# Optimization experiments

Hardware: AMD Instinct MI355X
Metric: run time of the kernel (lower is better)

Reference implementation:

```python
import jax, jax.numpy as jnp
import numpy as np

HEADS = 8
DIM_HEAD = 64
SCALE = DIM_HEAD ** -0.5


def setup_inputs() -> dict:
    key = jax.random.key(0)
    k1, k2, k3 = jax.random.split(key, 3)
    B, N, D = 4, 2048, HEADS * DIM_HEAD  # D = inner_dim = 512
    x = jax.random.normal(k1, (B, N, D), dtype=jnp.float32)
    # nn.Linear weights stored transposed vs torch; here we use [in, out]
    w_qkv = jax.random.normal(k2, (D, 3 * D), dtype=jnp.float32) * (D ** -0.5)
    w_out = jax.random.normal(k3, (D, D), dtype=jnp.float32) * (D ** -0.5)
    b_out = jnp.zeros((D,), dtype=jnp.float32)
    return {"x": x, "w_qkv": w_qkv, "w_out": w_out, "b_out": b_out}


def reference(x, w_qkv, w_out, b_out):
    B, N, D = x.shape
    qkv = x @ w_qkv  # [B, N, 3D]
    q, k, v = jnp.split(qkv, 3, axis=-1)

    def to_heads(t):  # b n (h d) -> b h n d
        return t.reshape(B, N, HEADS, DIM_HEAD).transpose(0, 2, 1, 3)

    q, k, v = to_heads(q), to_heads(k), to_heads(v)
    dots = jnp.einsum('bhnd,bhmd->bhnm', q, k) * SCALE  # [B,H,N,N]
    attn = jax.nn.softmax(dots, axis=-1)
    out = jnp.einsum('bhnm,bhmd->bhnd', attn, v)  # [B,H,N,d]
    out = out.transpose(0, 2, 1, 3).reshape(B, N, D)  # b h n d -> b n (h d)
    return out @ w_out + b_out
```

## Files before the change

kernel.cpp:

```cpp
#include <hip/hip_runtime.h>

typedef __bf16 bf16;
typedef __bf16 bf16x8 __attribute__((ext_vector_type(8)));
typedef __bf16 bf16x4 __attribute__((ext_vector_type(4)));
typedef float f32x4 __attribute__((ext_vector_type(4)));
typedef float f32x16 __attribute__((ext_vector_type(16)));

#define MFMA16(a, b, c) __builtin_amdgcn_mfma_f32_16x16x32_bf16(a, b, c, 0, 0, 0)
#define MFMA32(a, b, c) __builtin_amdgcn_mfma_f32_32x32x16_bf16(a, b, c, 0, 0, 0)

#define CS 0.18033688011112042f

#if __has_builtin(__builtin_amdgcn_exp2f)
#define EXP2(x) __builtin_amdgcn_exp2f(x)
#else
#define EXP2(x) exp2f(x)
#endif

__device__ __forceinline__ void load_lds16(const bf16* g, bf16* l) {
    __builtin_amdgcn_global_load_lds(
        (const __attribute__((address_space(1))) unsigned int*)g,
        (__attribute__((address_space(3))) unsigned int*)l, 16, 0, 0);
}

__device__ __forceinline__ bf16x4 shfl_xor32_b64(bf16x4 v) {
    union { bf16x4 b; int i[2]; } u;
    u.b = v;
    u.i[0] = __shfl_xor(u.i[0], 32, 64);
    u.i[1] = __shfl_xor(u.i[1], 32, 64);
    return u.b;
}

__device__ __forceinline__ bf16x8 build_bfrag(bf16x4 plo, bf16x4 phi, int h) {
    bf16x4 xlo = shfl_xor32_b64(plo);
    bf16x4 xhi = shfl_xor32_b64(phi);
    bf16x4 lo4 = h ? xhi : plo;
    bf16x4 hi4 = h ? phi : xlo;
    bf16x8 bb;
#pragma unroll
    for (int i = 0; i < 4; ++i) { bb[i] = lo4[i]; bb[4 + i] = hi4[i]; }
    return bb;
}

__global__ __launch_bounds__(256) void f32_to_bf16_kernel(const float* __restrict__ in,
                                                          bf16* __restrict__ out, int n) {
    int i = (blockIdx.x * 256 + threadIdx.x) * 4;
    if (i < n) {
        float4 v = *(const float4*)&in[i];
        bf16x4 o = {(bf16)v.x, (bf16)v.y, (bf16)v.z, (bf16)v.w};
        *(bf16x4*)&out[i] = o;
    }
}

__global__ __launch_bounds__(256) void transpose_f2b(const float* __restrict__ in,
                                                     bf16* __restrict__ out,
                                                     int R, int C) {
    __shared__ float tile[32][33];
    int tx = threadIdx.x & 31, ty = threadIdx.x >> 5;
    int c0 = blockIdx.x * 32, r0 = blockIdx.y * 32;
#pragma unroll
    for (int i = ty; i < 32; i += 8)
        tile[i][tx] = in[(size_t)(r0 + i) * C + c0 + tx];
    __syncthreads();
#pragma unroll
    for (int i = ty; i < 32; i += 8)
        out[(size_t)(c0 + i) * R + r0 + tx] = (bf16)tile[tx][i];
}

__global__ __launch_bounds__(256) void transpose_v_kernel(const bf16* __restrict__ qkv,
                                                          bf16* __restrict__ vt) {
    __shared__ bf16 tile[32][33];
    int tx = threadIdx.x & 31, ty = threadIdx.x >> 5;
    int bh = blockIdx.z, b = bh >> 3, h = bh & 7;
    int n0 = blockIdx.x * 32, d0 = blockIdx.y * 32;
#pragma unroll
    for (int i = ty; i < 32; i += 8)
        tile[i][tx] = qkv[(size_t)(b * 2048 + n0 + i) * 1536 + 1024 + h * 64 + d0 + tx];
    __syncthreads();
#pragma unroll
    for (int i = ty; i < 32; i += 8)
        vt[(size_t)(bh * 64 + d0 + i) * 2048 + n0 + tx] = tile[tx][i];
}

template <int MT, int MODE, typename OutT>
__global__ __launch_bounds__(256, 4) void gemm_bt_kernel(const bf16* __restrict__ A,
                                                         const bf16* __restrict__ Bt,
                                                         const float* __restrict__ bias,
                                                         OutT* __restrict__ C,
                                                         int M, int N, int K) {
    const int BM = MT * 32;
    __shared__ bf16 As[BM * 64];
    __shared__ bf16 Bs[128 * 64];
    int t = threadIdx.x;
    int lane = t & 63, w = t >> 6;
    int wr = w >> 1, wc = w & 1;
    int quad = lane >> 4, r16 = lane & 15;
    int m0 = blockIdx.y * BM, n0 = blockIdx.x * 128;

    const f32x4 fzero = {0.f, 0.f, 0.f, 0.f};
    f32x4 acc[MT][4];
#pragma unroll
    for (int i = 0; i < MT; ++i)
#pragma unroll
        for (int j = 0; j < 4; ++j) acc[i][j] = fzero;

    const bf16* ap[MT]; bf16* ad[MT];
    const bf16* bp[4];  bf16* bd[4];
#pragma unroll
    for (int i = 0; i < MT; ++i) {
        int ci = i * 256 + t;
        int row = ci >> 3, cp = ci & 7, cc = cp ^ (row & 7);
        ap[i] = &A[(size_t)(m0 + row) * K + cc * 8];
        ad[i] = &As[ci * 8];
    }
#pragma unroll
    for (int i = 0; i < 4; ++i) {
        int ci = i * 256 + t;
        int row = ci >> 3, cp = ci & 7, cc = cp ^ (row & 7);
        bp[i] = &Bt[(size_t)(n0 + row) * K + cc * 8];
        bd[i] = &Bs[ci * 8];
    }

    for (int k0 = 0; k0 < K; k0 += 64) {
        __syncthreads();
#pragma unroll
        for (int i = 0; i < MT; ++i) { load_lds16(ap[i], ad[i]); ap[i] += 64; }
#pragma unroll
        for (int i = 0; i < 4; ++i) { load_lds16(bp[i], bd[i]); bp[i] += 64; }
        __syncthreads();
#pragma unroll
        for (int ks = 0; ks < 2; ++ks) {
            bf16x8 af[MT], bfr[4];
            int cp = (ks * 4 + quad) ^ (r16 & 7);
#pragma unroll
            for (int mt = 0; mt < MT; ++mt)
                af[mt] = *(const bf16x8*)&As[(wr * (BM / 2) + mt * 16 + r16) * 64 + cp * 8];
#pragma unroll
            for (int nt = 0; nt < 4; ++nt)
                bfr[nt] = *(const bf16x8*)&Bs[(wc * 64 + nt * 16 + r16) * 64 + cp * 8];
#pragma unroll
            for (int mt = 0; mt < MT; ++mt)
#pragma unroll
                for (int nt = 0; nt < 4; ++nt)
                    acc[mt][nt] = MFMA16(af[mt], bfr[nt], acc[mt][nt]);
        }
    }
#pragma unroll
    for (int mt = 0; mt < MT; ++mt)
#pragma unroll
        for (int nt = 0; nt < 4; ++nt)
#pragma unroll
            for (int r = 0; r < 4; ++r) {
                int row = m0 + wr * (BM / 2) + mt * 16 + quad * 4 + r;
                int col = n0 + wc * 64 + nt * 16 + r16;
                float v = acc[mt][nt][r];
                if (MODE == 1 && n0 < 512) v *= CS;
                if (MODE == 2) v += bias[col];
                C[(size_t)row * N + col] = (OutT)v;
            }
}

__global__ __launch_bounds__(256, 2) void attn_kernel(const bf16* __restrict__ qkv,
                                                      const bf16* __restrict__ vt,
                                                      bf16* __restrict__ out) {
    __shared__ bf16 smem[16384];

    int t = threadIdx.x;
    int lane = t & 63, w = t >> 6;
    int h = lane >> 5, q = lane & 31;
    int g = w >> 1, wq = w & 1;
    int tt = t & 127;
    int bh = blockIdx.y, b = bh >> 3, hd = bh & 7;
    int qb = blockIdx.x * 64;
    int qrow = qb + wq * 32 + q;

    bf16x8 qf[4];
    {
        size_t qoff = (size_t)(b * 2048 + qrow) * 1536 + hd * 64;
#pragma unroll
        for (int s = 0; s < 4; ++s)
            qf[s] = *(const bf16x8*)&qkv[qoff + s * 16 + h * 8];
    }
    bf16x8 ones;
#pragma unroll
    for (int i = 0; i < 8; ++i) ones[i] = (bf16)1.0f;

    f32x16 o_acc[2], lacc;
#pragma unroll
    for (int i = 0; i < 16; ++i) { o_acc[0][i] = 0.f; o_acc[1][i] = 0.f; lacc[i] = 0.f; }

    bf16* Ks = &smem[g * 8192];
    bf16* Vs = Ks + 4096;

    const bf16* kp[4]; const bf16* vp[4];
    bf16* kd[4]; bf16* vd[4];
#pragma unroll
    for (int rdd = 0; rdd < 4; ++rdd) {
        int ci = rdd * 128 + tt;
        int row = ci >> 3, cp = ci & 7, cc = cp ^ (row & 7);
        kp[rdd] = &qkv[(size_t)(b * 2048 + g * 1024 + row) * 1536 + 512 + hd * 64 + cc * 8];
        kd[rdd] = &Ks[ci * 8];
        vp[rdd] = &vt[(size_t)(bh * 64 + row) * 2048 + g * 1024 + cc * 8];
        vd[rdd] = &Vs[ci * 8];
    }

    for (int it = 0; it < 16; ++it) {
        __syncthreads();
#pragma unroll
        for (int rdd = 0; rdd < 4; ++rdd) {
            load_lds16(kp[rdd], kd[rdd]); kp[rdd] += (size_t)64 * 1536;
            load_lds16(vp[rdd], vd[rdd]); vp[rdd] += 64;
        }
        __syncthreads();

        f32x16 sacc[2];
#pragma unroll
        for (int kb = 0; kb < 2; ++kb)
#pragma unroll
            for (int i = 0; i < 16; ++i) sacc[kb][i] = 0.f;

#pragma unroll
        for (int kb = 0; kb < 2; ++kb) {
            int m = kb * 32 + q;
#pragma unroll
            for (int s = 0; s < 4; ++s) {
                int cp = (s * 2 + h) ^ (q & 7);
                bf16x8 kf = *(const bf16x8*)&Ks[m * 64 + cp * 8];
                sacc[kb] = MFMA32(kf, qf[s], sacc[kb]);
            }
        }

        bf16x8 bfr[4];
#pragma unroll
        for (int kb = 0; kb < 2; ++kb) {
            bf16x4 pk[4];
#pragma unroll
            for (int g8 = 0; g8 < 4; ++g8)
#pragma unroll
                for (int i = 0; i < 4; ++i)
                    pk[g8][i] = (bf16)EXP2(sacc[kb][4 * g8 + i]);
#pragma unroll
            for (int wi = 0; wi < 2; ++wi)
                bfr[kb * 2 + wi] = build_bfrag(pk[2 * wi], pk[2 * wi + 1], h);
        }

#pragma unroll
        for (int j = 0; j < 4; ++j) lacc = MFMA32(ones, bfr[j], lacc);

#pragma unroll
        for (int kstep = 0; kstep < 4; ++kstep)
#pragma unroll
            for (int db = 0; db < 2; ++db) {
                int d = db * 32 + q;
                int cp = (kstep * 2 + h) ^ (q & 7);
                bf16x8 vf = *(const bf16x8*)&Vs[d * 64 + cp * 8];
                o_acc[db] = MFMA32(vf, bfr[kstep], o_acc[db]);
            }
    }

    float l_own = __shfl(lacc[0], q, 64);

    __syncthreads();
    float* Of = (float*)smem;
    float* Lf = (float*)(smem + 8192);
    bf16*  Ot = smem + 8320;

    if (g == 1) {
#pragma unroll
        for (int db = 0; db < 2; ++db)
#pragma unroll
            for (int g8 = 0; g8 < 4; ++g8)
#pragma unroll
                for (int i = 0; i < 4; ++i)
                    Of[(wq * 64 + db * 32 + g8 * 8 + h * 4 + i) * 32 + q] =
                        o_acc[db][g8 * 4 + i];
        if (h == 0) Lf[wq * 32 + q] = l_own;
    }
    __syncthreads();
    if (g == 0) {
        float linv = 1.f / (l_own + Lf[wq * 32 + q]);
#pragma unroll
        for (int db = 0; db < 2; ++db)
#pragma unroll
            for (int g8 = 0; g8 < 4; ++g8) {
                bf16x4 ov;
#pragma unroll
                for (int i = 0; i < 4; ++i)
                    ov[i] = (bf16)((o_acc[db][g8 * 4 + i] +
                                    Of[(wq * 64 + db * 32 + g8 * 8 + h * 4 + i) * 32 + q]) *
                                   linv);
                *(bf16x4*)&Ot[(wq * 32 + q) * 72 + db * 32 + g8 * 8 + h * 4] = ov;
            }
    }
    __syncthreads();
#pragma unroll
    for (int rnd = 0; rnd < 2; ++rnd) {
        int idx = rnd * 256 + t;
        int row = idx >> 3, col = (idx & 7) * 8;
        bf16x8 ov = *(const bf16x8*)&Ot[row * 72 + col];
        *(bf16x8*)&out[(size_t)(b * 2048 + qb + row) * 512 + hd * 64 + col] = ov;
    }
}

extern "C" void kernel_launch(void* const* d_in, const int* in_sizes, int n_in,
                              void* d_out, int out_size, void* d_ws, size_t ws_size,
                              hipStream_t stream) {
    const float* x     = (const float*)d_in[0];
    const float* w_qkv = (const float*)d_in[1];
    const float* w_out = (const float*)d_in[2];
    const float* b_out = (const float*)d_in[3];
    float* out = (float*)d_out;

    char* ws = (char*)d_ws;
    size_t off = 0;
    bf16* xb    = (bf16*)(ws + off); off += (size_t)8192 * 512 * 2;
    bf16* wqkvT = (bf16*)(ws + off); off += (size_t)1536 * 512 * 2;
    bf16* woutT = (bf16*)(ws + off); off += (size_t)512 * 512 * 2;
    bf16* qkv   = (bf16*)(ws + off); off += (size_t)8192 * 1536 * 2;
    bf16* vt    = (bf16*)(ws + off); off += (size_t)32 * 64 * 2048 * 2;
    bf16* attn  = (bf16*)(ws + off);

    f32_to_bf16_kernel<<<4096, 256, 0, stream>>>(x, xb, 8192 * 512);
    transpose_f2b<<<dim3(48, 16), 256, 0, stream>>>(w_qkv, wqkvT, 512, 1536);
    transpose_f2b<<<dim3(16, 16), 256, 0, stream>>>(w_out, woutT, 512, 512);
    gemm_bt_kernel<2, 1, bf16><<<dim3(12, 128), 256, 0, stream>>>(
        xb, wqkvT, nullptr, qkv, 8192, 1536, 512);
    transpose_v_kernel<<<dim3(64, 2, 32), 256, 0, stream>>>(qkv, vt);
    attn_kernel<<<dim3(32, 32), 256, 0, stream>>>(qkv, vt, attn);
    gemm_bt_kernel<2, 2, float><<<dim3(4, 128), 256, 0, stream>>>(
        attn, woutT, b_out, out, 8192, 512, 512);
}
```

Before: 183.9 us.

## Restructure attention into per-wave private K/V staging without block barriers

The attention kernel drops from four waves to two. Each wave owns its own LDS staging buffer and streams half of the keys in 32-key chunks, waiting on its own vector-memory counter instead of a block-wide barrier. Each wave now covers both 32-row query sub-tiles, so one K/V fragment load serves two sets of MFMAs. The row sum is accumulated in scalar registers instead of through an extra ones-matrix MFMA, and the two key halves are merged through LDS in the epilogue. The QKV GEMM also moves to a 128-row tile with matching launch bounds. This trades block synchronisation and the redundant MFMA for fewer waves per block, more registers per wave and an unbuffered load-then-compute loop with no overlap.

```diff
diff --git a/kernel.cpp b/kernel.cpp
--- a/kernel.cpp
+++ b/kernel.cpp
@@ -16,6 +16,8 @@
 #else
 #define EXP2(x) exp2f(x)
 #endif
+
+#define WAIT_VM0() __builtin_amdgcn_s_waitcnt(0x0F70)
 
 __device__ __forceinline__ void load_lds16(const bf16* g, bf16* l) {
     __builtin_amdgcn_global_load_lds(
@@ -83,11 +85,12 @@
 }
 
 template <int MT, int MODE, typename OutT>
-__global__ __launch_bounds__(256, 4) void gemm_bt_kernel(const bf16* __restrict__ A,
-                                                         const bf16* __restrict__ Bt,
-                                                         const float* __restrict__ bias,
-                                                         OutT* __restrict__ C,
-                                                         int M, int N, int K) {
+__global__ __launch_bounds__(256, (MT == 4) ? 2 : 4)
+void gemm_bt_kernel(const bf16* __restrict__ A,
+                    const bf16* __restrict__ Bt,
+                    const float* __restrict__ bias,
+                    OutT* __restrict__ C,
+                    int M, int N, int K) {
     const int BM = MT * 32;
     __shared__ bf16 As[BM * 64];
     __shared__ bf16 Bs[128 * 64];
@@ -160,145 +163,162 @@
             }
 }
 
-__global__ __launch_bounds__(256, 2) void attn_kernel(const bf16* __restrict__ qkv,
+__global__ __launch_bounds__(128, 2) void attn_kernel(const bf16* __restrict__ qkv,
                                                       const bf16* __restrict__ vt,
                                                       bf16* __restrict__ out) {
-    __shared__ bf16 smem[16384];
+    __shared__ __align__(16) char smemraw[18432];
+    bf16* stage = (bf16*)smemraw;
 
     int t = threadIdx.x;
     int lane = t & 63, w = t >> 6;
     int h = lane >> 5, q = lane & 31;
-    int g = w >> 1, wq = w & 1;
-    int tt = t & 127;
     int bh = blockIdx.y, b = bh >> 3, hd = bh & 7;
     int qb = blockIdx.x * 64;
-    int qrow = qb + wq * 32 + q;
-
-    bf16x8 qf[4];
-    {
-        size_t qoff = (size_t)(b * 2048 + qrow) * 1536 + hd * 64;
+
+    bf16x8 qf[2][4];
+#pragma unroll
+    for (int sub = 0; sub < 2; ++sub) {
+        size_t qoff = (size_t)(b * 2048 + qb + sub * 32 + q) * 1536 + hd * 64;
 #pragma unroll
         for (int s = 0; s < 4; ++s)
-            qf[s] = *(const bf16x8*)&qkv[qoff + s * 16 + h * 8];
-    }
-    bf16x8 ones;
-#pragma unroll
-    for (int i = 0; i < 8; ++i) ones[i] = (bf16)1.0f;
-
-    f32x16 o_acc[2], lacc;
-#pragma unroll
-    for (int i = 0; i < 16; ++i) { o_acc[0][i] = 0.f; o_acc[1][i] = 0.f; lacc[i] = 0.f; }
-
-    bf16* Ks = &smem[g * 8192];
-    bf16* Vs = Ks + 4096;
+            qf[sub][s] = *(const bf16x8*)&qkv[qoff + s * 16 + h * 8];
+    }
+
+    f32x16 o_acc[2][2];
+#pragma unroll
+    for (int sub = 0; sub < 2; ++sub)
+#pragma unroll
+        for (int db = 0; db < 2; ++db)
+#pragma unroll
+            for (int i = 0; i < 16; ++i) o_acc[sub][db][i] = 0.f;
+    float psum[2] = {0.f, 0.f};
+
+    bf16* Ks = stage + w * 4096;
+    bf16* Vs = Ks + 2048;
 
     const bf16* kp[4]; const bf16* vp[4];
     bf16* kd[4]; bf16* vd[4];
 #pragma unroll
     for (int rdd = 0; rdd < 4; ++rdd) {
-        int ci = rdd * 128 + tt;
-        int row = ci >> 3, cp = ci & 7, cc = cp ^ (row & 7);
-        kp[rdd] = &qkv[(size_t)(b * 2048 + g * 1024 + row) * 1536 + 512 + hd * 64 + cc * 8];
-        kd[rdd] = &Ks[ci * 8];
-        vp[rdd] = &vt[(size_t)(bh * 64 + row) * 2048 + g * 1024 + cc * 8];
-        vd[rdd] = &Vs[ci * 8];
-    }
-
-    for (int it = 0; it < 16; ++it) {
-        __syncthreads();
+        int ciK = rdd * 64 + lane;
+        int rowK = ciK >> 3, ccK = (ciK & 7) ^ (rowK & 7);
+        kp[rdd] = &qkv[(size_t)(b * 2048 + w * 1024 + rowK) * 1536 + 512 + hd * 64 + ccK * 8];
+        kd[rdd] = &Ks[ciK * 8];
+        int ciV = rdd * 64 + lane;
+        int rowV = ciV >> 2, ccV = (ciV & 3) ^ (rowV & 3);
+        vp[rdd] = &vt[(size_t)(bh * 64 + rowV) * 2048 + w * 1024 + ccV * 8];
+        vd[rdd] = &Vs[ciV * 8];
+    }
+
+    for (int it = 0; it < 32; ++it) {
 #pragma unroll
         for (int rdd = 0; rdd < 4; ++rdd) {
-            load_lds16(kp[rdd], kd[rdd]); kp[rdd] += (size_t)64 * 1536;
-            load_lds16(vp[rdd], vd[rdd]); vp[rdd] += 64;
-        }
-        __syncthreads();
-
-        f32x16 sacc[2];
-#pragma unroll
-        for (int kb = 0; kb < 2; ++kb)
-#pragma unroll
-            for (int i = 0; i < 16; ++i) sacc[kb][i] = 0.f;
-
-#pragma unroll
-        for (int kb = 0; kb < 2; ++kb) {
-            int m = kb * 32 + q;
-#pragma unroll
-            for (int s = 0; s < 4; ++s) {
-                int cp = (s * 2 + h) ^ (q & 7);
-                bf16x8 kf = *(const bf16x8*)&Ks[m * 64 + cp * 8];
-                sacc[kb] = MFMA32(kf, qf[s], sacc[kb]);
+            load_lds16(kp[rdd], kd[rdd]); kp[rdd] += (size_t)32 * 1536;
+            load_lds16(vp[rdd], vd[rdd]); vp[rdd] += 32;
+        }
+        WAIT_VM0();
+
+        bf16x8 kf[4];
+#pragma unroll
+        for (int s = 0; s < 4; ++s) {
+            int cp = (s * 2 + h) ^ (q & 7);
+            kf[s] = *(const bf16x8*)&Ks[q * 64 + cp * 8];
+        }
+        bf16x8 vf[2][2];
+#pragma unroll
+        for (int kstep = 0; kstep < 2; ++kstep)
+#pragma unroll
+            for (int db = 0; db < 2; ++db) {
+                int cp = (kstep * 2 + h) ^ (q & 3);
+                vf[kstep][db] = *(const bf16x8*)&Vs[(db * 32 + q) * 32 + cp * 8];
             }
-        }
-
-        bf16x8 bfr[4];
-#pragma unroll
-        for (int kb = 0; kb < 2; ++kb) {
+
+#pragma unroll
+        for (int sub = 0; sub < 2; ++sub) {
+            f32x16 sacc;
+#pragma unroll
+            for (int i = 0; i < 16; ++i) sacc[i] = 0.f;
+#pragma unroll
+            for (int s = 0; s < 4; ++s)
+                sacc = MFMA32(kf[s], qf[sub][s], sacc);
+
             bf16x4 pk[4];
+            float ps = 0.f;
 #pragma unroll
             for (int g8 = 0; g8 < 4; ++g8)
 #pragma unroll
-                for (int i = 0; i < 4; ++i)
-                    pk[g8][i] = (bf16)EXP2(sacc[kb][4 * g8 + i]);
-#pragma unroll
-            for (int wi = 0; wi < 2; ++wi)
-                bfr[kb * 2 + wi] = build_bfrag(pk[2 * wi], pk[2 * wi + 1], h);
-        }
-
-#pragma unroll
-        for (int j = 0; j < 4; ++j) lacc = MFMA32(ones, bfr[j], lacc);
-
-#pragma unroll
-        for (int kstep = 0; kstep < 4; ++kstep)
+                for (int i = 0; i < 4; ++i) {
+                    float p = EXP2(sacc[4 * g8 + i]);
+                    ps += p;
+                    pk[g8][i] = (bf16)p;
+                }
+            psum[sub] += ps;
+            bf16x8 bfr0 = build_bfrag(pk[0], pk[1], h);
+            bf16x8 bfr1 = build_bfrag(pk[2], pk[3], h);
+
 #pragma unroll
             for (int db = 0; db < 2; ++db) {
-                int d = db * 32 + q;
-                int cp = (kstep * 2 + h) ^ (q & 7);
-                bf16x8 vf = *(const bf16x8*)&Vs[d * 64 + cp * 8];
-                o_acc[db] = MFMA32(vf, bfr[kstep], o_acc[db]);
+                o_acc[sub][db] = MFMA32(vf[0][db], bfr0, o_acc[sub][db]);
+                o_acc[sub][db] = MFMA32(vf[1][db], bfr1, o_acc[sub][db]);
             }
-    }
-
-    float l_own = __shfl(lacc[0], q, 64);
-
-    __syncthreads();
-    float* Of = (float*)smem;
-    float* Lf = (float*)(smem + 8192);
-    bf16*  Ot = smem + 8320;
-
-    if (g == 1) {
-#pragma unroll
-        for (int db = 0; db < 2; ++db)
-#pragma unroll
-            for (int g8 = 0; g8 < 4; ++g8)
-#pragma unroll
-                for (int i = 0; i < 4; ++i)
-                    Of[(wq * 64 + db * 32 + g8 * 8 + h * 4 + i) * 32 + q] =
-                        o_acc[db][g8 * 4 + i];
-        if (h == 0) Lf[wq * 32 + q] = l_own;
-    }
-    __syncthreads();
-    if (g == 0) {
-        float linv = 1.f / (l_own + Lf[wq * 32 + q]);
-#pragma unroll
-        for (int db = 0; db < 2; ++db)
-#pragma unroll
-            for (int g8 = 0; g8 < 4; ++g8) {
-                bf16x4 ov;
-#pragma unroll
-                for (int i = 0; i < 4; ++i)
-                    ov[i] = (bf16)((o_acc[db][g8 * 4 + i] +
-                                    Of[(wq * 64 + db * 32 + g8 * 8 + h * 4 + i) * 32 + q]) *
-                                   linv);
-                *(bf16x4*)&Ot[(wq * 32 + q) * 72 + db * 32 + g8 * 8 + h * 4] = ov;
+        }
+    }
+
+    float l_own[2];
+#pragma unroll
+    for (int sub = 0; sub < 2; ++sub)
+        l_own[sub] = psum[sub] + __shfl_xor(psum[sub], 32, 64);
+
+    __syncthreads();
+    float* Of = (float*)smemraw;
+    float* Lf = (float*)(smemraw + 17408);
+
+    if (w == 1) {
+#pragma unroll
+        for (int sub = 0; sub < 2; ++sub) {
+#pragma unroll
+            for (int db = 0; db < 2; ++db)
+#pragma unroll
+                for (int r = 0; r < 16; ++r) {
+                    int d = db * 32 + (r & 3) + 8 * (r >> 2) + 4 * h;
+                    Of[(sub * 32 + q) * 68 + d] = o_acc[sub][db][r];
+                }
+            if (h == 0) Lf[sub * 32 + q] = l_own[sub];
+        }
+    }
+    __syncthreads();
+    if (w == 0) {
+#pragma unroll
+        for (int sub = 0; sub < 2; ++sub) {
+#pragma unroll
+            for (int db = 0; db < 2; ++db)
+#pragma unroll
+                for (int r = 0; r < 16; ++r) {
+                    int d = db * 32 + (r & 3) + 8 * (r >> 2) + 4 * h;
+                    Of[(sub * 32 + q) * 68 + d] += o_acc[sub][db][r];
+                }
+            if (h == 0) Lf[sub * 32 + q] += l_own[sub];
+        }
+    }
+    __syncthreads();
+
+    {
+        int row = t >> 1, half = t & 1;
+        float linv = 1.f / Lf[row];
+        const float* src = &Of[row * 68 + half * 32];
+        bf16* dst = &out[(size_t)(b * 2048 + qb + row) * 512 + hd * 64 + half * 32];
+#pragma unroll
+        for (int i = 0; i < 4; ++i) {
+            f32x4 a = *(const f32x4*)&src[i * 8];
+            f32x4 c = *(const f32x4*)&src[i * 8 + 4];
+            bf16x8 o8;
+#pragma unroll
+            for (int j = 0; j < 4; ++j) {
+                o8[j] = (bf16)(a[j] * linv);
+                o8[4 + j] = (bf16)(c[j] * linv);
             }
-    }
-    __syncthreads();
-#pragma unroll
-    for (int rnd = 0; rnd < 2; ++rnd) {
-        int idx = rnd * 256 + t;
-        int row = idx >> 3, col = (idx & 7) * 8;
-        bf16x8 ov = *(const bf16x8*)&Ot[row * 72 + col];
-        *(bf16x8*)&out[(size_t)(b * 2048 + qb + row) * 512 + hd * 64 + col] = ov;
+            *(bf16x8*)&dst[i * 8] = o8;
+        }
     }
 }
 
@@ -323,10 +343,10 @@
     f32_to_bf16_kernel<<<4096, 256, 0, stream>>>(x, xb, 8192 * 512);
     transpose_f2b<<<dim3(48, 16), 256, 0, stream>>>(w_qkv, wqkvT, 512, 1536);
     transpose_f2b<<<dim3(16, 16), 256, 0, stream>>>(w_out, woutT, 512, 512);
-    gemm_bt_kernel<2, 1, bf16><<<dim3(12, 128), 256, 0, stream>>>(
+    gemm_bt_kernel<4, 1, bf16><<<dim3(12, 64), 256, 0, stream>>>(
         xb, wqkvT, nullptr, qkv, 8192, 1536, 512);
     transpose_v_kernel<<<dim3(64, 2, 32), 256, 0, stream>>>(qkv, vt);
-    attn_kernel<<<dim3(32, 32), 256, 0, stream>>>(qkv, vt, attn);
+    attn_kernel<<<dim3(32, 32), 128, 0, stream>>>(qkv, vt, attn);
     gemm_bt_kernel<2, 2, float><<<dim3(4, 128), 256, 0, stream>>>(
         attn, woutT, b_out, out, 8192, 512, 512);
 }
```

After: 170.9 us. -7.0%, faster.
